# Kernel tuning notes

Measured on AMD Instinct MI355X. Metric: run time of the kernel, lower is better.

Reference implementation:

```python
import jax, jax.numpy as jnp
import numpy as np

BINS = 30
MOMENTUM = 0.75
LOSS_WEIGHT = 1.0


def setup_inputs() -> dict:
    key = jax.random.key(0)
    k1, k2 = jax.random.split(key)
    N, C = 8192, 2048
    preds = jax.random.normal(k1, (N, C), dtype=jnp.float32)
    targets = jax.random.randint(k2, (N, C), 0, 2).astype(jnp.int32)  # binary multi-hot
    acc_sum = jnp.zeros((BINS, C), dtype=jnp.float32)  # EMA histogram state
    return {"preds": preds, "targets": targets, "acc_sum": acc_sum}


def reference(preds, targets, acc_sum):
    N, C = preds.shape
    t = targets.astype(preds.dtype)

    # gradient norm g = |sigmoid(p) - t|, detached (weights carry no grad)
    g = jnp.abs(jax.nn.sigmoid(jax.lax.stop_gradient(preds)) - t)

    # bin index: edges[i] = i/BINS, so bin = floor(g*BINS), g=1.0 -> last bin (edge[-1]+=1e-6)
    bin_idx = jnp.clip(jnp.floor(g * BINS).astype(jnp.int32), 0, BINS - 1)  # [N, C]

    # per-label histogram: counts[b, c] = #examples with bin b in column c
    cols = jnp.broadcast_to(jnp.arange(C, dtype=jnp.int32)[None, :], (N, C))
    counts = jnp.zeros((BINS, C), dtype=preds.dtype).at[bin_idx, cols].add(1.0)

    # n[c] = number of non-empty bins for label c
    n = jnp.sum(counts >= 1.0, axis=0).astype(preds.dtype)  # [C]

    # EMA update of the histogram (momentum > 0 branch)
    acc_new = MOMENTUM * acc_sum + (1.0 - MOMENTUM) * counts  # [BINS, C]

    tot = jnp.asarray(float(max(N, 1.0)), preds.dtype)
    weights = tot / acc_new[bin_idx, cols]               # gather per-element density
    weights = weights / jnp.maximum(n, 1.0)[None, :]      # normalize by #valid bins
    weights = jax.lax.stop_gradient(weights)

    # BCE with logits, elementwise: softplus-style stable form
    bce = jnp.logaddexp(0.0, preds) - preds * t
    loss = jnp.mean(weights * bce)
    return loss * LOSS_WEIGHT
```

## Files before the change

kernel.cpp:

```cpp
#include <hip/hip_runtime.h>

#define BINS  30
#define NROWS 8192
#define NCOLS 2048
#define COLS_PER_BLK 256
#define ROWS_PER_BLK 128
#define YSLICES 64

#define FIXED_SCALE 16384.0f
#define CNT_SHIFT   24
#define SUM_MASK    ((1u << CNT_SHIFT) - 1)

#define WS_PART  0
#define WS_CNT   (YSLICES * BINS * NCOLS * 4)
#define WS_BSUM  (WS_CNT + BINS * NCOLS * 4)
#define WS_BPART (WS_BSUM + BINS * NCOLS * 4)
#define WS_CTR   (WS_BPART + 8 * 4)

__global__ __launch_bounds__(256, 5) void k_main(
    const float* __restrict__ preds, const int* __restrict__ targets,
    unsigned int* __restrict__ part, unsigned int* __restrict__ ctr)
{
    __shared__ unsigned int H[BINS * COLS_PER_BLK];
    const int t = threadIdx.x;
    if (blockIdx.x == 0 && blockIdx.y == 0 && t == 0) atomicExch(ctr, 0u);
    #pragma unroll
    for (int i = 0; i < BINS; ++i) H[i * COLS_PER_BLK + t] = 0u;
    __syncthreads();

    const int col = blockIdx.x * COLS_PER_BLK + t;
    const int r0  = blockIdx.y * ROWS_PER_BLK;
    const float* P = preds   + (size_t)r0 * NCOLS + col;
    const int*   T = targets + (size_t)r0 * NCOLS + col;

    float pc[8]; int tc[8];
    #pragma unroll
    for (int r = 0; r < 8; ++r) { pc[r] = P[r * NCOLS]; tc[r] = T[r * NCOLS]; }

    #pragma unroll 1
    for (int batch = 0; batch < ROWS_PER_BLK / 8; ++batch) {
        float pn[8]; int tn[8];
        if (batch < ROWS_PER_BLK / 8 - 1) {
            P += 8 * NCOLS; T += 8 * NCOLS;
            #pragma unroll
            for (int r = 0; r < 8; ++r) { pn[r] = P[r * NCOLS]; tn[r] = T[r * NCOLS]; }
        }
        __builtin_amdgcn_sched_barrier(0);

        #pragma unroll
        for (int r = 0; r < 8; ++r) {
            float p  = pc[r];
            float pp = tc[r] ? -p : p;
            float e  = __expf(-fabsf(pp));
            float d  = 1.0f + e;
            float r1 = __builtin_amdgcn_rcpf(d);
            float g  = (pp >= 0.0f) ? r1 : e * r1;
            int   b  = (int)(g * 30.0f);
            b = b > (BINS - 1) ? (BINS - 1) : b;
            float bce = fmaxf(pp, 0.0f) + __logf(d);
            unsigned int pk = (1u << CNT_SHIFT)
                | (unsigned int)(bce * FIXED_SCALE + 0.5f);
            H[b * COLS_PER_BLK + t] += pk;
        }
        #pragma unroll
        for (int r = 0; r < 8; ++r) { pc[r] = pn[r]; tc[r] = tn[r]; }
    }
    __syncthreads();

    const size_t outBase = (size_t)blockIdx.y * BINS * NCOLS
                         + (size_t)blockIdx.x * COLS_PER_BLK;
    for (int i = t; i < BINS * COLS_PER_BLK; i += 256)
        part[outBase + (size_t)(i >> 8) * NCOLS + (i & 255)] = H[i];
}

__global__ __launch_bounds__(256) void k_reduce(
    const unsigned int* __restrict__ part,
    float* __restrict__ cnt_f, float* __restrict__ bsum_f)
{
    const int id = blockIdx.x * 256 + threadIdx.x;
    unsigned int cnt = 0u, sm = 0u;
    #pragma unroll 16
    for (int y = 0; y < YSLICES; ++y) {
        const unsigned int v = part[(size_t)y * BINS * NCOLS + id];
        cnt += v >> CNT_SHIFT;
        sm  += v & SUM_MASK;
    }
    cnt_f[id]  = (float)cnt;
    bsum_f[id] = (float)sm * (1.0f / FIXED_SCALE);
}

__global__ __launch_bounds__(256) void k_colsum(
    const float* __restrict__ cnt_f, const float* __restrict__ bsum_f,
    const float* __restrict__ acc_sum, float* __restrict__ blockPart,
    unsigned int* __restrict__ ctr, float* __restrict__ out)
{
    __shared__ float wave_sums[4];
    const int tid = threadIdx.x;
    const int c   = blockIdx.x * 256 + tid;

    float colsum = 0.0f;
    int n = 0;
    #pragma unroll
    for (int b = 0; b < BINS; ++b) {
        const size_t gidx = (size_t)b * NCOLS + c;
        const float cnt = cnt_f[gidx];
        if (cnt >= 1.0f) {
            n += 1;
            float acc_new = 0.75f * acc_sum[gidx] + 0.25f * cnt;
            colsum += bsum_f[gidx] / acc_new;
        }
    }
    colsum /= (float)((n > 1 ? n : 1) * NCOLS);

    #pragma unroll
    for (int off = 32; off > 0; off >>= 1)
        colsum += __shfl_down(colsum, off, 64);
    if ((tid & 63) == 0) wave_sums[tid >> 6] = colsum;
    __syncthreads();
    if (tid == 0) {
        const float s = wave_sums[0] + wave_sums[1] + wave_sums[2] + wave_sums[3];
        atomicExch(&blockPart[blockIdx.x], s);
        __threadfence();
        if (atomicAdd(ctr, 1u) == 7u) {
            __threadfence();
            double d = 0.0;
            #pragma unroll
            for (int i = 0; i < 8; ++i)
                d += (double)atomicAdd(&blockPart[i], 0.0f);
            out[0] = (float)d;
        }
    }
}

extern "C" void kernel_launch(void* const* d_in, const int* in_sizes, int n_in,
                              void* d_out, int out_size, void* d_ws, size_t ws_size,
                              hipStream_t stream)
{
    const float* preds   = (const float*)d_in[0];
    const int*   targets = (const int*)d_in[1];
    const float* acc_sum = (const float*)d_in[2];

    unsigned int* part = (unsigned int*)((char*)d_ws + WS_PART);
    float* cnt_f       = (float*)((char*)d_ws + WS_CNT);
    float* bsum_f      = (float*)((char*)d_ws + WS_BSUM);
    float* blockPart   = (float*)((char*)d_ws + WS_BPART);
    unsigned int* ctr  = (unsigned int*)((char*)d_ws + WS_CTR);

    dim3 gA(NCOLS / COLS_PER_BLK, NROWS / ROWS_PER_BLK);
    k_main<<<gA, 256, 0, stream>>>(preds, targets, part, ctr);

    k_reduce<<<(BINS * NCOLS) / 256, 256, 0, stream>>>(part, cnt_f, bsum_f);

    k_colsum<<<NCOLS / 256, 256, 0, stream>>>(cnt_f, bsum_f, acc_sum,
                                              blockPart, ctr, (float*)d_out);
}
```

Measured before the change: 183.1 us.

## Fuse slice reduction and column sum into one tail kernel

Merges the separate partial-histogram reduction kernel and the per-column weighting kernel into a single 8-block, 512-thread kernel. Each block owns 256 columns and splits the 64 row-slices between two thread halves, which combine through LDS. This removes one kernel launch and the float cnt/bsum intermediate arrays written to and re-read from global memory. In exchange, the whole 15.7 MB partial buffer is now read by only 8 workgroups, so the reduction may become badly under-parallelized on a device with many CUs.

```diff
diff --git a/kernel.cpp b/kernel.cpp
--- a/kernel.cpp
+++ b/kernel.cpp
@@ -12,9 +12,7 @@
 #define SUM_MASK    ((1u << CNT_SHIFT) - 1)
 
 #define WS_PART  0
-#define WS_CNT   (YSLICES * BINS * NCOLS * 4)
-#define WS_BSUM  (WS_CNT + BINS * NCOLS * 4)
-#define WS_BPART (WS_BSUM + BINS * NCOLS * 4)
+#define WS_BPART (YSLICES * BINS * NCOLS * 4)
 #define WS_CTR   (WS_BPART + 8 * 4)
 
 __global__ __launch_bounds__(256, 5) void k_main(
@@ -73,51 +71,71 @@
         part[outBase + (size_t)(i >> 8) * NCOLS + (i & 255)] = H[i];
 }
 
-__global__ __launch_bounds__(256) void k_reduce(
+__global__ __launch_bounds__(512) void k_tail(
     const unsigned int* __restrict__ part,
-    float* __restrict__ cnt_f, float* __restrict__ bsum_f)
+    const float* __restrict__ acc_sum,
+    float* __restrict__ blockPart, unsigned int* __restrict__ ctr,
+    float* __restrict__ out)
 {
-    const int id = blockIdx.x * 256 + threadIdx.x;
-    unsigned int cnt = 0u, sm = 0u;
-    #pragma unroll 16
-    for (int y = 0; y < YSLICES; ++y) {
-        const unsigned int v = part[(size_t)y * BINS * NCOLS + id];
-        cnt += v >> CNT_SHIFT;
-        sm  += v & SUM_MASK;
+    __shared__ unsigned int Lc[BINS * 256];
+    __shared__ unsigned int Ls[BINS * 256];
+    __shared__ float wave_sums[4];
+    const int t  = threadIdx.x;
+    const int cl = t & 255;
+    const int q  = t >> 8;
+    const int colBase = blockIdx.x * 256;
+
+    unsigned int cq[BINS], sq[BINS];
+    #pragma unroll
+    for (int b = 0; b < BINS; ++b) { cq[b] = 0u; sq[b] = 0u; }
+
+    const unsigned int* Pp = part + (size_t)(q * 32) * (BINS * NCOLS)
+                                  + colBase + cl;
+    #pragma unroll 1
+    for (int y = 0; y < 32; ++y) {
+        #pragma unroll
+        for (int b = 0; b < BINS; ++b) {
+            const unsigned int v = Pp[(size_t)b * NCOLS];
+            cq[b] += v >> CNT_SHIFT;
+            sq[b] += v & SUM_MASK;
+        }
+        Pp += BINS * NCOLS;
     }
-    cnt_f[id]  = (float)cnt;
-    bsum_f[id] = (float)sm * (1.0f / FIXED_SCALE);
-}
 
-__global__ __launch_bounds__(256) void k_colsum(
-    const float* __restrict__ cnt_f, const float* __restrict__ bsum_f,
-    const float* __restrict__ acc_sum, float* __restrict__ blockPart,
-    unsigned int* __restrict__ ctr, float* __restrict__ out)
-{
-    __shared__ float wave_sums[4];
-    const int tid = threadIdx.x;
-    const int c   = blockIdx.x * 256 + tid;
-
-    float colsum = 0.0f;
-    int n = 0;
-    #pragma unroll
-    for (int b = 0; b < BINS; ++b) {
-        const size_t gidx = (size_t)b * NCOLS + c;
-        const float cnt = cnt_f[gidx];
-        if (cnt >= 1.0f) {
-            n += 1;
-            float acc_new = 0.75f * acc_sum[gidx] + 0.25f * cnt;
-            colsum += bsum_f[gidx] / acc_new;
+    if (q == 1) {
+        #pragma unroll
+        for (int b = 0; b < BINS; ++b) {
+            Lc[b * 256 + cl] = cq[b];
+            Ls[b * 256 + cl] = sq[b];
         }
     }
-    colsum /= (float)((n > 1 ? n : 1) * NCOLS);
+    __syncthreads();
 
-    #pragma unroll
-    for (int off = 32; off > 0; off >>= 1)
-        colsum += __shfl_down(colsum, off, 64);
-    if ((tid & 63) == 0) wave_sums[tid >> 6] = colsum;
+    if (q == 0) {
+        const int c = colBase + cl;
+        float colsum = 0.0f;
+        int n = 0;
+        #pragma unroll
+        for (int b = 0; b < BINS; ++b) {
+            const unsigned int cu = cq[b] + Lc[b * 256 + cl];
+            const unsigned int su = sq[b] + Ls[b * 256 + cl];
+            const float cnt = (float)cu;
+            if (cnt >= 1.0f) {
+                n += 1;
+                float acc_new = 0.75f * acc_sum[(size_t)b * NCOLS + c] + 0.25f * cnt;
+                colsum += ((float)su * (1.0f / FIXED_SCALE)) / acc_new;
+            }
+        }
+        colsum /= (float)((n > 1 ? n : 1) * NCOLS);
+
+        #pragma unroll
+        for (int off = 32; off > 0; off >>= 1)
+            colsum += __shfl_down(colsum, off, 64);
+        if ((t & 63) == 0) wave_sums[t >> 6] = colsum;
+    }
     __syncthreads();
-    if (tid == 0) {
+
+    if (t == 0) {
         const float s = wave_sums[0] + wave_sums[1] + wave_sums[2] + wave_sums[3];
         atomicExch(&blockPart[blockIdx.x], s);
         __threadfence();
@@ -141,16 +159,11 @@
     const float* acc_sum = (const float*)d_in[2];
 
     unsigned int* part = (unsigned int*)((char*)d_ws + WS_PART);
-    float* cnt_f       = (float*)((char*)d_ws + WS_CNT);
-    float* bsum_f      = (float*)((char*)d_ws + WS_BSUM);
     float* blockPart   = (float*)((char*)d_ws + WS_BPART);
     unsigned int* ctr  = (unsigned int*)((char*)d_ws + WS_CTR);
 
     dim3 gA(NCOLS / COLS_PER_BLK, NROWS / ROWS_PER_BLK);
     k_main<<<gA, 256, 0, stream>>>(preds, targets, part, ctr);
 
-    k_reduce<<<(BINS * NCOLS) / 256, 256, 0, stream>>>(part, cnt_f, bsum_f);
-
-    k_colsum<<<NCOLS / 256, 256, 0, stream>>>(cnt_f, bsum_f, acc_sum,
-                                              blockPart, ctr, (float*)d_out);
+    k_tail<<<8, 512, 0, stream>>>(part, acc_sum, blockPart, ctr, (float*)d_out);
 }
```

Result: slower. 202.3 us (+10.5%).
